# Kernel optimization log

Hardware: AMD Instinct MI355X
Metric: run time of the kernel (lower is better)

## Reference

```python
import jax, jax.numpy as jnp
import numpy as np

C = 128  # in_dim

def _proj(x, w, b):
    # 1x1 conv: x [b,c,h,w], w [out,in], b [out] -> [b,out,h*w]
    bsz, c, h, wd = x.shape
    y = jnp.einsum('bchw,oc->bohw', x, w) + b[None, :, None, None]
    return y.reshape(bsz, -1, h * wd)

def setup_inputs() -> dict:
    key = jax.random.key(0)
    ks = jax.random.split(key, 7)
    x = jax.random.normal(ks[0], (16, C, 128, 128), dtype=jnp.float32)
    s = 1.0 / np.sqrt(C)
    qw = jax.random.normal(ks[1], (C, C), dtype=jnp.float32) * s
    kw = jax.random.normal(ks[2], (C, C), dtype=jnp.float32) * s
    vw = jax.random.normal(ks[3], (C, C), dtype=jnp.float32) * s
    qb = jax.random.normal(ks[4], (C,), dtype=jnp.float32) * 0.01
    kb = jax.random.normal(ks[5], (C,), dtype=jnp.float32) * 0.01
    vb = jax.random.normal(ks[6], (C,), dtype=jnp.float32) * 0.01
    return {'x': x, 'qw': qw, 'qb': qb, 'kw': kw, 'kb': kb, 'vw': vw, 'vb': vb}

def reference(x, qw, qb, kw, kb, vw, vb):
    x_s, x_t = jnp.split(x, 2, axis=0)
    b, c, h, w = x_s.shape
    q_s = _proj(x_s, qw, qb); q_t = _proj(x_t, qw, qb)   # [b,c,N]
    k_s = _proj(x_s, kw, kb); k_t = _proj(x_t, kw, kb)   # [b,c,N]
    v_s = _proj(x_s, vw, vb); v_t = _proj(x_t, vw, vb)   # [b,c,N]
    # channel cross-attentions: contract over spatial N -> [b,c,c]
    a_st = jax.nn.softmax(jnp.einsum('bcn,bdn->bcd', q_t, k_s), axis=-1)
    a_ts = jax.nn.softmax(jnp.einsum('bcn,bdn->bcd', q_s, k_t), axis=-1)
    att = jax.nn.softmax(jnp.einsum('bce,bde->bcd', a_st, a_ts), axis=-1)
    out_s = jnp.einsum('bcd,bdn->bcn', att, v_s).reshape(b, c, h, w)
    out_t = jnp.einsum('bcd,bdn->bcn', att, v_t).reshape(b, c, h, w)
    return jnp.concatenate((x_s + out_s, x_t + out_t), axis=0)
```

## Files before the change

### kernel.cpp

```cpp
#include <hip/hip_runtime.h>
#include <hip/hip_bf16.h>

#define CC 128
#define NSP 16384
#define NFULL (CC * NSP)

typedef float f32x4 __attribute__((ext_vector_type(4)));
typedef short s16x8 __attribute__((ext_vector_type(8)));
typedef unsigned int u32x4 __attribute__((ext_vector_type(4)));

#define GLOAD16(g, l) __builtin_amdgcn_global_load_lds( \
    (const __attribute__((address_space(1))) void*)(g), \
    (__attribute__((address_space(3))) void*)(l), 16, 0, 0)

__device__ __forceinline__ unsigned bf16rne(float f) {
  unsigned u = __float_as_uint(f);
  return ((u + 0x7FFFu + ((u >> 16) & 1u)) >> 16) & 0xFFFFu;
}

__device__ __forceinline__ uint2 packpair(float x0, float x1) {
  __hip_bfloat162 h2 = __float22bfloat162_rn(make_float2(x0, x1));
  unsigned hu = *reinterpret_cast<unsigned*>(&h2);
  float hf0 = __uint_as_float(hu << 16);
  float hf1 = __uint_as_float(hu & 0xFFFF0000u);
  __hip_bfloat162 l2 = __float22bfloat162_rn(make_float2(x0 - hf0, x1 - hf1));
  unsigned lu = *reinterpret_cast<unsigned*>(&l2);
  return make_uint2(hu, lu);
}

__global__ __launch_bounds__(256) void zerok(float* __restrict__ p, int n) {
  int i = blockIdx.x * 256 + threadIdx.x;
  if (i < n) p[i] = 0.f;
}

__global__ __launch_bounds__(256, 2) void k1_mfma(const float* __restrict__ x,
    float* __restrict__ Mdst, float* __restrict__ rs, float* __restrict__ rt,
    float* __restrict__ rspart, float* __restrict__ rtpart,
    int nst, int mode) {
  const int b = blockIdx.y;
  const int chunk = blockIdx.x;
  const int n0 = chunk * (nst * 32);
  const int t = threadIdx.x;
  const int w = t >> 6, l = t & 63;
  const int wr = w >> 1, wc = w & 1;
  const int lr = l & 15, lg = l >> 4;
  __shared__ __align__(16) char LB[2][2][128 * 128];
  const float* Xs = x + (size_t)b * NFULL;
  const float* Xt = x + (size_t)(b + 8) * NFULL;
  const int srow0 = w * 32 + (l >> 3);
  const int sn16x = (l & 7);

  f32x4 acc[4][4];
#pragma unroll
  for (int a = 0; a < 4; ++a)
#pragma unroll
    for (int bb = 0; bb < 4; ++bb) acc[a][bb] = (f32x4){0.f, 0.f, 0.f, 0.f};
  float rtp[4] = {0.f, 0.f, 0.f, 0.f};
  float rsp[4] = {0.f, 0.f, 0.f, 0.f};

  {
#pragma unroll
    for (int i = 0; i < 4; ++i) {
      int row = srow0 + i * 8;
      int n16 = sn16x ^ (row & 7);
      GLOAD16(Xt + (size_t)row * NSP + n0 + n16 * 4, &LB[0][0][(w * 32 + i * 8) * 128]);
      GLOAD16(Xs + (size_t)row * NSP + n0 + n16 * 4, &LB[0][1][(w * 32 + i * 8) * 128]);
    }
  }

  for (int s = 0; s < nst; ++s) {
    const int cur = s & 1;
    __syncthreads();
    if (s + 1 < nst) {
      const int nb = n0 + (s + 1) * 32;
#pragma unroll
      for (int i = 0; i < 4; ++i) {
        int row = srow0 + i * 8;
        int n16 = sn16x ^ (row & 7);
        GLOAD16(Xt + (size_t)row * NSP + nb + n16 * 4, &LB[cur ^ 1][0][(w * 32 + i * 8) * 128]);
        GLOAD16(Xs + (size_t)row * NSP + nb + n16 * 4, &LB[cur ^ 1][1][(w * 32 + i * 8) * 128]);
      }
    }
    const char* A = &LB[cur][0][0];
    const char* B = &LB[cur][1][0];
    s16x8 ah[4], al[4], bh[4], bl[4];
#pragma unroll
    for (int a = 0; a < 4; ++a) {
      int row = wr * 64 + a * 16 + lr;
      int base = row * 128, sw = row & 7;
      f32x4 f0 = *(const f32x4*)(A + base + (((lg * 2) ^ sw) << 4));
      f32x4 f1 = *(const f32x4*)(A + base + (((lg * 2 + 1) ^ sw) << 4));
      rtp[a] += ((f0[0] + f0[1]) + (f0[2] + f0[3])) + ((f1[0] + f1[1]) + (f1[2] + f1[3]));
      uint2 p0 = packpair(f0[0], f0[1]);
      uint2 p1 = packpair(f0[2], f0[3]);
      uint2 p2 = packpair(f1[0], f1[1]);
      uint2 p3 = packpair(f1[2], f1[3]);
      u32x4 H = {p0.x, p1.x, p2.x, p3.x};
      u32x4 L = {p0.y, p1.y, p2.y, p3.y};
      ah[a] = __builtin_bit_cast(s16x8, H);
      al[a] = __builtin_bit_cast(s16x8, L);
    }
#pragma unroll
    for (int bb = 0; bb < 4; ++bb) {
      int row = wc * 64 + bb * 16 + lr;
      int base = row * 128, sw = row & 7;
      f32x4 f0 = *(const f32x4*)(B + base + (((lg * 2) ^ sw) << 4));
      f32x4 f1 = *(const f32x4*)(B + base + (((lg * 2 + 1) ^ sw) << 4));
      rsp[bb] += ((f0[0] + f0[1]) + (f0[2] + f0[3])) + ((f1[0] + f1[1]) + (f1[2] + f1[3]));
      uint2 p0 = packpair(f0[0], f0[1]);
      uint2 p1 = packpair(f0[2], f0[3]);
      uint2 p2 = packpair(f1[0], f1[1]);
      uint2 p3 = packpair(f1[2], f1[3]);
      u32x4 H = {p0.x, p1.x, p2.x, p3.x};
      u32x4 L = {p0.y, p1.y, p2.y, p3.y};
      bh[bb] = __builtin_bit_cast(s16x8, H);
      bl[bb] = __builtin_bit_cast(s16x8, L);
    }
#pragma unroll
    for (int a = 0; a < 4; ++a)
#pragma unroll
      for (int bb = 0; bb < 4; ++bb) {
        acc[a][bb] = __builtin_amdgcn_mfma_f32_16x16x32_bf16(ah[a], bh[bb], acc[a][bb], 0, 0, 0);
        acc[a][bb] = __builtin_amdgcn_mfma_f32_16x16x32_bf16(ah[a], bl[bb], acc[a][bb], 0, 0, 0);
        acc[a][bb] = __builtin_amdgcn_mfma_f32_16x16x32_bf16(al[a], bh[bb], acc[a][bb], 0, 0, 0);
      }
  }

#pragma unroll
  for (int a = 0; a < 4; ++a) {
    float vt = rtp[a];
    vt += __shfl_xor(vt, 16);
    vt += __shfl_xor(vt, 32);
    float vs = rsp[a];
    vs += __shfl_xor(vs, 16);
    vs += __shfl_xor(vs, 32);
    if (l < 16) {
      if (wc == 0) {
        int row = wr * 64 + a * 16 + l;
        if (mode == 0) rtpart[((size_t)chunk * 8 + b) * CC + row] = vt;
        else atomicAdd(&rt[b * CC + row], vt);
      }
      if (wr == 0) {
        int row = wc * 64 + a * 16 + l;
        if (mode == 0) rspart[((size_t)chunk * 8 + b) * CC + row] = vs;
        else atomicAdd(&rs[b * CC + row], vs);
      }
    }
  }

  const int rquad = lg << 2;
  if (mode == 0) {
    float* Mp = Mdst + ((size_t)chunk * 8 + b) * (CC * CC);
#pragma unroll
    for (int a = 0; a < 4; ++a)
#pragma unroll
      for (int bb = 0; bb < 4; ++bb)
#pragma unroll
        for (int r = 0; r < 4; ++r) {
          int i = wr * 64 + a * 16 + rquad + r;
          int j = wc * 64 + bb * 16 + lr;
          Mp[i * CC + j] = acc[a][bb][r];
        }
  } else {
    float* Mp = Mdst + (size_t)b * (CC * CC);
#pragma unroll
    for (int a = 0; a < 4; ++a)
#pragma unroll
      for (int bb = 0; bb < 4; ++bb)
#pragma unroll
        for (int r = 0; r < 4; ++r) {
          int i = wr * 64 + a * 16 + rquad + r;
          int j = wc * 64 + bb * 16 + lr;
          atomicAdd(&Mp[i * CC + j], acc[a][bb][r]);
        }
  }
}

__global__ __launch_bounds__(256) void k1_reduce(const float* __restrict__ Mpart,
    const float* __restrict__ rspart, const float* __restrict__ rtpart,
    float* __restrict__ M, float* __restrict__ rs, float* __restrict__ rt,
    int NB) {
  const int t = threadIdx.x;
  if (blockIdx.x < 128) {
    const int i4 = blockIdx.x * 256 + t;
    const int b = i4 >> 12;
    const int e = (i4 & 4095) * 4;
    f32x4 s = (f32x4){0.f, 0.f, 0.f, 0.f};
    for (int c = 0; c < NB; ++c) {
      f32x4 v = *(const f32x4*)(Mpart + ((size_t)c * 8 + b) * (CC * CC) + e);
      s += v;
    }
    *(f32x4*)(M + (size_t)b * CC * CC + e) = s;
  } else if (blockIdx.x == 128) {
    const int e = t * 4;
    f32x4 s = (f32x4){0.f, 0.f, 0.f, 0.f};
    for (int c = 0; c < NB; ++c) s += *(const f32x4*)(rtpart + (size_t)c * 1024 + e);
    *(f32x4*)(rt + e) = s;
  } else {
    const int e = t * 4;
    f32x4 s = (f32x4){0.f, 0.f, 0.f, 0.f};
    for (int c = 0; c < NB; ++c) s += *(const f32x4*)(rspart + (size_t)c * 1024 + e);
    *(f32x4*)(rs + e) = s;
  }
}

__global__ __launch_bounds__(256) void k2ab(const float* __restrict__ M,
    const float* __restrict__ qw, const float* __restrict__ kw,
    const float* __restrict__ qb, const float* __restrict__ kb,
    const float* __restrict__ rs, const float* __restrict__ rt,
    float* __restrict__ Ast, float* __restrict__ Ats) {
  const int b = blockIdx.y;
  const int c0 = blockIdx.x * 8;
  __shared__ float Big[128][132];
  __shared__ float Wq[8][128];
  __shared__ float T12[2][8][128];
  __shared__ float uvv[2][8];
  __shared__ float wv2[2][128];
  const int t = threadIdx.x;
  const float* Mb = M + (size_t)b * CC * CC;
#pragma unroll
  for (int p = 0; p < 16; ++p) {
    int f = p * 256 + t;
    int row = f >> 5, c4 = (f & 31) * 4;
    *(f32x4*)&Big[row][c4] = *(const f32x4*)(Mb + row * CC + c4);
  }
  { int row = t >> 5, c4 = (t & 31) * 4;
    *(f32x4*)&Wq[row][c4] = *(const f32x4*)(qw + (c0 + row) * CC + c4); }
  __syncthreads();
  if (t < 16) {
    int c = t & 7;
    const float* r = ((t < 8) ? rs : rt) + b * CC;
    float s = 0.f;
    for (int i = 0; i < CC; ++i) s += Wq[c][i] * r[i];
    uvv[(t < 8) ? 1 : 0][c] = s;
  }
  const int tr = t >> 5;
  const int L = t & 31;
  {
    float a1[4] = {0.f, 0.f, 0.f, 0.f}, a2[4] = {0.f, 0.f, 0.f, 0.f};
    for (int i = 0; i < CC; ++i) {
      float wq = Wq[tr][i];
#pragma unroll
      for (int j = 0; j < 4; ++j) a1[j] += wq * Big[i][L + 32 * j];
    }
    for (int i4 = 0; i4 < 32; ++i4) {
      f32x4 wq4 = *(const f32x4*)&Wq[tr][i4 * 4];
#pragma unroll
      for (int j = 0; j < 4; ++j) {
        f32x4 m4 = *(const f32x4*)&Big[L + 32 * j][i4 * 4];
        a2[j] += wq4[0]*m4[0] + wq4[1]*m4[1] + wq4[2]*m4[2] + wq4[3]*m4[3];
      }
    }
#pragma unroll
    for (int j = 0; j < 4; ++j) {
      T12[0][tr][L + 32 * j] = a1[j];
      T12[1][tr][L + 32 * j] = a2[j];
    }
  }
  __syncthreads();
#pragma unroll
  for (int p = 0; p < 16; ++p) {
    int f = p * 256 + t;
    int row = f >> 5, c4 = (f & 31) * 4;
    *(f32x4*)&Big[row][c4] = *(const f32x4*)(kw + row * CC + c4);
  }
  __syncthreads();
  {
    int d = t & 127, wh = t >> 7;
    const float* r = (wh ? rt : rs) + b * CC;
    float s = 0.f;
    for (int i4 = 0; i4 < 32; ++i4) {
      f32x4 w4 = *(const f32x4*)&Big[d][i4 * 4];
      s += w4[0]*r[i4*4] + w4[1]*r[i4*4+1] + w4[2]*r[i4*4+2] + w4[3]*r[i4*4+3];
    }
    wv2[wh][d] = s;
  }
  __syncthreads();
  const int c = c0 + tr;
  const float bqc = qb[c];
#pragma unroll 1
  for (int which = 0; which < 2; ++which) {
    float g[4];
#pragma unroll
    for (int j = 0; j < 4; ++j) {
      int d = L + 32 * j;
      g[j] = uvv[which][tr] * kb[d] + bqc * wv2[which][d] + 16384.f * bqc * kb[d];
    }
    for (int j4 = 0; j4 < 32; ++j4) {
      f32x4 tv4 = *(const f32x4*)&T12[which][tr][j4 * 4];
#pragma unroll
      for (int j = 0; j < 4; ++j) {
        f32x4 w4 = *(const f32x4*)&Big[L + 32 * j][j4 * 4];
        g[j] += tv4[0]*w4[0] + tv4[1]*w4[1] + tv4[2]*w4[2] + tv4[3]*w4[3];
      }
    }
    float m = fmaxf(fmaxf(g[0], g[1]), fmaxf(g[2], g[3]));
#pragma unroll
    for (int off = 1; off < 32; off <<= 1) m = fmaxf(m, __shfl_xor(m, off));
    float s = 0.f;
#pragma unroll
    for (int j = 0; j < 4; ++j) { g[j] = expf(g[j] - m); s += g[j]; }
#pragma unroll
    for (int off = 1; off < 32; off <<= 1) s += __shfl_xor(s, off);
    const float inv = 1.f / s;
    float* A = (which ? Ats : Ast) + (size_t)b * CC * CC + (size_t)c * CC;
#pragma unroll
    for (int j = 0; j < 4; ++j) A[L + 32 * j] = g[j] * inv;
  }
}

__global__ __launch_bounds__(256) void k2cd(const float* __restrict__ Ast,
    const float* __restrict__ Ats, const float* __restrict__ vw,
    const float* __restrict__ vb, unsigned short* __restrict__ Pbf,
    float* __restrict__ c0v) {
  const int b = blockIdx.y;
  const int c0 = blockIdx.x * 8;
  __shared__ float Big[128][132];
  __shared__ float Tl[8][128];
  __shared__ float Al[8][128];
  const int t = threadIdx.x;
  const float* Bb = Ats + (size_t)b * CC * CC;
  const float* Tb = Ast + (size_t)b * CC * CC;
#pragma unroll
  for (int p = 0; p < 16; ++p) {
    int f = p * 256 + t;
    int row = f >> 5, c4 = (f & 31) * 4;
    *(f32x4*)&Big[row][c4] = *(const f32x4*)(Bb + row * CC + c4);
  }
  { int row = t >> 5, c4 = (t & 31) * 4;
    *(f32x4*)&Tl[row][c4] = *(const f32x4*)(Tb + (c0 + row) * CC + c4); }
  __syncthreads();
  const int tr = t >> 5;
  const int L = t & 31;
  {
    float g[4] = {0.f, 0.f, 0.f, 0.f};
    for (int e4 = 0; e4 < 32; ++e4) {
      f32x4 tv4 = *(const f32x4*)&Tl[tr][e4 * 4];
#pragma unroll
      for (int j = 0; j < 4; ++j) {
        f32x4 a4 = *(const f32x4*)&Big[L + 32 * j][e4 * 4];
        g[j] += tv4[0]*a4[0] + tv4[1]*a4[1] + tv4[2]*a4[2] + tv4[3]*a4[3];
      }
    }
    float m = fmaxf(fmaxf(g[0], g[1]), fmaxf(g[2], g[3]));
#pragma unroll
    for (int off = 1; off < 32; off <<= 1) m = fmaxf(m, __shfl_xor(m, off));
    float s = 0.f;
#pragma unroll
    for (int j = 0; j < 4; ++j) { g[j] = expf(g[j] - m); s += g[j]; }
#pragma unroll
    for (int off = 1; off < 32; off <<= 1) s += __shfl_xor(s, off);
    const float inv = 1.f / s;
#pragma unroll
    for (int j = 0; j < 4; ++j) Al[tr][L + 32 * j] = g[j] * inv;
  }
  __syncthreads();
#pragma unroll
  for (int p = 0; p < 16; ++p) {
    int f = p * 256 + t;
    int row = f >> 5, c4 = (f & 31) * 4;
    *(f32x4*)&Big[row][c4] = *(const f32x4*)(vw + row * CC + c4);
  }
  __syncthreads();
  float p4[4] = {0.f, 0.f, 0.f, 0.f};
  for (int d = 0; d < CC; ++d) {
    float av = Al[tr][d];
#pragma unroll
    for (int j = 0; j < 4; ++j) p4[j] += av * Big[d][L + 32 * j];
  }
  float csum = 0.f;
#pragma unroll
  for (int j = 0; j < 4; ++j) csum += Al[tr][L + 32 * j] * vb[L + 32 * j];
#pragma unroll
  for (int off = 1; off < 32; off <<= 1) csum += __shfl_xor(csum, off);
  const int c = c0 + tr;
  if ((c & 31) == L) p4[c >> 5] += 1.0f;
  unsigned short* Pp = Pbf + (size_t)b * CC * CC + (size_t)c * CC;
#pragma unroll
  for (int j = 0; j < 4; ++j) Pp[L + 32 * j] = (unsigned short)bf16rne(p4[j]);
  if (L == 0) c0v[b * CC + c] = csum;
}

__global__ __launch_bounds__(256, 2) void k3_mfma(const float* __restrict__ x,
    const unsigned short* __restrict__ Pbf, const float* __restrict__ c0v,
    float* __restrict__ out) {
  const int im = blockIdx.y;
  const int pb = im & 7;
  const int n0 = blockIdx.x * 256;
  const float* X = x + (size_t)im * NFULL;
  float* O = out + (size_t)im * NFULL;
  __shared__ unsigned short XT[256 * 128];
  __shared__ float c0l[128];
  const int t = threadIdx.x;
  const int w = t >> 6, l = t & 63;
  const int ln = l & 15, lg = l >> 4;
  if (t < 128) c0l[t] = c0v[pb * CC + t];
#pragma unroll
  for (int p = 0; p < 16; ++p) {
    int d0 = 2 * (t >> 4) + 32 * (p & 3);
    int n4 = (t & 15) * 4 + 64 * (p >> 2);
    f32x4 x0 = *(const f32x4*)(X + (size_t)d0 * NSP + n0 + n4);
    f32x4 x1 = *(const f32x4*)(X + (size_t)(d0 + 1) * NSP + n0 + n4);
#pragma unroll
    for (int i = 0; i < 4; ++i) {
      int n = n4 + i;
      __hip_bfloat162 h2 = __float22bfloat162_rn(make_float2(x0[i], x1[i]));
      unsigned pk = *reinterpret_cast<unsigned*>(&h2);
      int g = ((((n & 3) << 1) ^ ((n >> 2) & 7)) << 4);
      int off = (n * 256 + d0 * 2) ^ g;
      *(unsigned*)((char*)XT + off) = pk;
    }
  }
  const unsigned short* Pg0 = Pbf + (size_t)pb * (CC * CC) + (size_t)ln * CC + lg * 8;
  s16x8 Af0[4][4];
#pragma unroll
  for (int a = 0; a < 4; ++a)
#pragma unroll
    for (int kk = 0; kk < 4; ++kk)
      Af0[a][kk] = *(const s16x8*)(Pg0 + a * 16 * CC + kk * 32);
  __syncthreads();

#pragma unroll
  for (int h = 0; h < 2; ++h) {
    s16x8 Af[4][4];
    if (h == 0) {
#pragma unroll
      for (int a = 0; a < 4; ++a)
#pragma unroll
        for (int kk = 0; kk < 4; ++kk) Af[a][kk] = Af0[a][kk];
    } else {
      const unsigned short* Pg = Pg0 + (size_t)64 * CC;
#pragma unroll
      for (int a = 0; a < 4; ++a)
#pragma unroll
        for (int kk = 0; kk < 4; ++kk)
          Af[a][kk] = *(const s16x8*)(Pg + a * 16 * CC + kk * 32);
    }
#pragma unroll
    for (int sub = 0; sub < 4; ++sub) {
      int row = sub * 64 + w * 16 + ln;
      int g = ((((row & 3) << 1) ^ ((row >> 2) & 7)) << 4);
      s16x8 bf[4];
#pragma unroll
      for (int kk = 0; kk < 4; ++kk)
        bf[kk] = *(const s16x8*)((char*)XT + ((row * 256 + kk * 64 + lg * 16) ^ g));
      f32x4 acc[4];
#pragma unroll
      for (int a = 0; a < 4; ++a) acc[a] = (f32x4){0.f, 0.f, 0.f, 0.f};
#pragma unroll
      for (int kk = 0; kk < 4; ++kk)
#pragma unroll
        for (int a = 0; a < 4; ++a)
          acc[a] = __builtin_amdgcn_mfma_f32_16x16x32_bf16(Af[a][kk], bf[kk], acc[a], 0, 0, 0);
      int n = n0 + sub * 64 + w * 16 + ln;
#pragma unroll
      for (int a = 0; a < 4; ++a)
#pragma unroll
        for (int r = 0; r < 4; ++r) {
          int c = h * 64 + a * 16 + lg * 4 + r;
          __builtin_nontemporal_store(acc[a][r] + c0l[c], O + (size_t)c * NSP + n);
        }
    }
  }
}

extern "C" void kernel_launch(void* const* d_in, const int* in_sizes, int n_in,
                              void* d_out, int out_size, void* d_ws, size_t ws_size,
                              hipStream_t stream) {
  (void)in_sizes; (void)n_in; (void)out_size;
  const float* x  = (const float*)d_in[0];
  const float* qw = (const float*)d_in[1];
  const float* qb = (const float*)d_in[2];
  const float* kw = (const float*)d_in[3];
  const float* kb = (const float*)d_in[4];
  const float* vw = (const float*)d_in[5];
  const float* vb = (const float*)d_in[6];
  float* out = (float*)d_out;
  float* ws = (float*)d_ws;
  float* M   = ws;
  float* rs  = M + 131072;
  float* rt  = rs + 1024;
  float* AST = rt + 1024;
  float* ATS = AST + 131072;
  unsigned short* Pbf = (unsigned short*)(ATS + 131072);
  float* c0v = ATS + 131072 + 65536;
  float* Mpart = c0v + 1024;
  const size_t base_floats = (size_t)(Mpart - ws);

  int NB, mode;
  if (ws_size >= (base_floats + (size_t)32 * (131072 + 2048)) * 4) { NB = 32; mode = 0; }
  else { NB = 32; mode = 1; }
  const int nst = (16384 / NB) / 32;
  float* rtpart = Mpart + (size_t)NB * 131072;
  float* rspart = rtpart + (size_t)NB * 1024;

  if (mode == 1) zerok<<<(133120 + 255) / 256, 256, 0, stream>>>(M, 133120);
  k1_mfma<<<dim3(NB, 8), 256, 0, stream>>>(x, mode ? M : Mpart, rs, rt,
                                           rspart, rtpart, nst, mode);
  if (mode == 0)
    k1_reduce<<<130, 256, 0, stream>>>(Mpart, rspart, rtpart, M, rs, rt, NB);
  k2ab<<<dim3(16, 8), 256, 0, stream>>>(M, qw, kw, qb, kb, rs, rt, AST, ATS);
  k2cd<<<dim3(16, 8), 256, 0, stream>>>(AST, ATS, vw, vb, Pbf, c0v);
  k3_mfma<<<dim3(64, 16), 256, 0, stream>>>(x, Pbf, c0v, out);
}
```

Before: 137.2 us.

## Halve rows per block in k2ab/k2cd and vectorize k3 output stores via swapped MFMA

k2ab and k2cd now handle 4 channel rows per block instead of 8, using 64 lanes per row and doubling the grid to 256 blocks so more CUs are busy in these small stages. Each block still loads the full 128x128 matrices, so total global and LDS traffic for those loads doubles. Separately, k3_mfma swaps the MFMA operand order so each lane holds 4 consecutive spatial outputs for one channel. This lets the output be written with one 16-byte nontemporal vector store per accumulator instead of four scalar stores.

```diff
diff --git a/kernel.cpp b/kernel.cpp
--- a/kernel.cpp
+++ b/kernel.cpp
@@ -210,11 +210,11 @@
     const float* __restrict__ rs, const float* __restrict__ rt,
     float* __restrict__ Ast, float* __restrict__ Ats) {
   const int b = blockIdx.y;
-  const int c0 = blockIdx.x * 8;
+  const int c0 = blockIdx.x * 4;
   __shared__ float Big[128][132];
-  __shared__ float Wq[8][128];
-  __shared__ float T12[2][8][128];
-  __shared__ float uvv[2][8];
+  __shared__ float Wq[4][128];
+  __shared__ float T12[2][4][128];
+  __shared__ float uvv[2][4];
   __shared__ float wv2[2][128];
   const int t = threadIdx.x;
   const float* Mb = M + (size_t)b * CC * CC;
@@ -224,37 +224,39 @@
     int row = f >> 5, c4 = (f & 31) * 4;
     *(f32x4*)&Big[row][c4] = *(const f32x4*)(Mb + row * CC + c4);
   }
-  { int row = t >> 5, c4 = (t & 31) * 4;
-    *(f32x4*)&Wq[row][c4] = *(const f32x4*)(qw + (c0 + row) * CC + c4); }
-  __syncthreads();
-  if (t < 16) {
-    int c = t & 7;
-    const float* r = ((t < 8) ? rs : rt) + b * CC;
+  if (t < 128) {
+    int row = t >> 5, c4 = (t & 31) * 4;
+    *(f32x4*)&Wq[row][c4] = *(const f32x4*)(qw + (c0 + row) * CC + c4);
+  }
+  __syncthreads();
+  if (t < 8) {
+    int c = t & 3;
+    const float* r = ((t < 4) ? rs : rt) + b * CC;
     float s = 0.f;
     for (int i = 0; i < CC; ++i) s += Wq[c][i] * r[i];
-    uvv[(t < 8) ? 1 : 0][c] = s;
-  }
-  const int tr = t >> 5;
-  const int L = t & 31;
+    uvv[(t < 4) ? 1 : 0][c] = s;
+  }
+  const int tr = t >> 6;
+  const int L = t & 63;
   {
-    float a1[4] = {0.f, 0.f, 0.f, 0.f}, a2[4] = {0.f, 0.f, 0.f, 0.f};
+    float a1[2] = {0.f, 0.f}, a2[2] = {0.f, 0.f};
     for (int i = 0; i < CC; ++i) {
       float wq = Wq[tr][i];
 #pragma unroll
-      for (int j = 0; j < 4; ++j) a1[j] += wq * Big[i][L + 32 * j];
+      for (int j = 0; j < 2; ++j) a1[j] += wq * Big[i][L + 64 * j];
     }
     for (int i4 = 0; i4 < 32; ++i4) {
       f32x4 wq4 = *(const f32x4*)&Wq[tr][i4 * 4];
 #pragma unroll
-      for (int j = 0; j < 4; ++j) {
-        f32x4 m4 = *(const f32x4*)&Big[L + 32 * j][i4 * 4];
+      for (int j = 0; j < 2; ++j) {
+        f32x4 m4 = *(const f32x4*)&Big[L + 64 * j][i4 * 4];
         a2[j] += wq4[0]*m4[0] + wq4[1]*m4[1] + wq4[2]*m4[2] + wq4[3]*m4[3];
       }
     }
 #pragma unroll
-    for (int j = 0; j < 4; ++j) {
-      T12[0][tr][L + 32 * j] = a1[j];
-      T12[1][tr][L + 32 * j] = a2[j];
+    for (int j = 0; j < 2; ++j) {
+      T12[0][tr][L + 64 * j] = a1[j];
+      T12[1][tr][L + 64 * j] = a2[j];
     }
   }
   __syncthreads();
@@ -280,32 +282,31 @@
   const float bqc = qb[c];
 #pragma unroll 1
   for (int which = 0; which < 2; ++which) {
-    float g[4];
-#pragma unroll
-    for (int j = 0; j < 4; ++j) {
-      int d = L + 32 * j;
+    float g[2];
+#pragma unroll
+    for (int j = 0; j < 2; ++j) {
+      int d = L + 64 * j;
       g[j] = uvv[which][tr] * kb[d] + bqc * wv2[which][d] + 16384.f * bqc * kb[d];
     }
     for (int j4 = 0; j4 < 32; ++j4) {
       f32x4 tv4 = *(const f32x4*)&T12[which][tr][j4 * 4];
 #pragma unroll
-      for (int j = 0; j < 4; ++j) {
-        f32x4 w4 = *(const f32x4*)&Big[L + 32 * j][j4 * 4];
+      for (int j = 0; j < 2; ++j) {
+        f32x4 w4 = *(const f32x4*)&Big[L + 64 * j][j4 * 4];
         g[j] += tv4[0]*w4[0] + tv4[1]*w4[1] + tv4[2]*w4[2] + tv4[3]*w4[3];
       }
     }
-    float m = fmaxf(fmaxf(g[0], g[1]), fmaxf(g[2], g[3]));
-#pragma unroll
-    for (int off = 1; off < 32; off <<= 1) m = fmaxf(m, __shfl_xor(m, off));
-    float s = 0.f;
-#pragma unroll
-    for (int j = 0; j < 4; ++j) { g[j] = expf(g[j] - m); s += g[j]; }
-#pragma unroll
-    for (int off = 1; off < 32; off <<= 1) s += __shfl_xor(s, off);
+    float m = fmaxf(g[0], g[1]);
+#pragma unroll
+    for (int off = 1; off < 64; off <<= 1) m = fmaxf(m, __shfl_xor(m, off));
+    float s = g[0] = expf(g[0] - m);
+    s += (g[1] = expf(g[1] - m));
+#pragma unroll
+    for (int off = 1; off < 64; off <<= 1) s += __shfl_xor(s, off);
     const float inv = 1.f / s;
     float* A = (which ? Ats : Ast) + (size_t)b * CC * CC + (size_t)c * CC;
-#pragma unroll
-    for (int j = 0; j < 4; ++j) A[L + 32 * j] = g[j] * inv;
+    A[L] = g[0] * inv;
+    A[L + 64] = g[1] * inv;
   }
 }
 
@@ -314,10 +315,10 @@
     const float* __restrict__ vb, unsigned short* __restrict__ Pbf,
     float* __restrict__ c0v) {
   const int b = blockIdx.y;
-  const int c0 = blockIdx.x * 8;
+  const int c0 = blockIdx.x * 4;
   __shared__ float Big[128][132];
-  __shared__ float Tl[8][128];
-  __shared__ float Al[8][128];
+  __shared__ float Tl[4][128];
+  __shared__ float Al[4][128];
   const int t = threadIdx.x;
   const float* Bb = Ats + (size_t)b * CC * CC;
   const float* Tb = Ast + (size_t)b * CC * CC;
@@ -327,32 +328,33 @@
     int row = f >> 5, c4 = (f & 31) * 4;
     *(f32x4*)&Big[row][c4] = *(const f32x4*)(Bb + row * CC + c4);
   }
-  { int row = t >> 5, c4 = (t & 31) * 4;
-    *(f32x4*)&Tl[row][c4] = *(const f32x4*)(Tb + (c0 + row) * CC + c4); }
-  __syncthreads();
-  const int tr = t >> 5;
-  const int L = t & 31;
+  if (t < 128) {
+    int row = t >> 5, c4 = (t & 31) * 4;
+    *(f32x4*)&Tl[row][c4] = *(const f32x4*)(Tb + (c0 + row) * CC + c4);
+  }
+  __syncthreads();
+  const int tr = t >> 6;
+  const int L = t & 63;
   {
-    float g[4] = {0.f, 0.f, 0.f, 0.f};
+    float g[2] = {0.f, 0.f};
     for (int e4 = 0; e4 < 32; ++e4) {
       f32x4 tv4 = *(const f32x4*)&Tl[tr][e4 * 4];
 #pragma unroll
-      for (int j = 0; j < 4; ++j) {
-        f32x4 a4 = *(const f32x4*)&Big[L + 32 * j][e4 * 4];
+      for (int j = 0; j < 2; ++j) {
+        f32x4 a4 = *(const f32x4*)&Big[L + 64 * j][e4 * 4];
         g[j] += tv4[0]*a4[0] + tv4[1]*a4[1] + tv4[2]*a4[2] + tv4[3]*a4[3];
       }
     }
-    float m = fmaxf(fmaxf(g[0], g[1]), fmaxf(g[2], g[3]));
-#pragma unroll
-    for (int off = 1; off < 32; off <<= 1) m = fmaxf(m, __shfl_xor(m, off));
-    float s = 0.f;
-#pragma unroll
-    for (int j = 0; j < 4; ++j) { g[j] = expf(g[j] - m); s += g[j]; }
-#pragma unroll
-    for (int off = 1; off < 32; off <<= 1) s += __shfl_xor(s, off);
+    float m = fmaxf(g[0], g[1]);
+#pragma unroll
+    for (int off = 1; off < 64; off <<= 1) m = fmaxf(m, __shfl_xor(m, off));
+    float s = g[0] = expf(g[0] - m);
+    s += (g[1] = expf(g[1] - m));
+#pragma unroll
+    for (int off = 1; off < 64; off <<= 1) s += __shfl_xor(s, off);
     const float inv = 1.f / s;
-#pragma unroll
-    for (int j = 0; j < 4; ++j) Al[tr][L + 32 * j] = g[j] * inv;
+    Al[tr][L] = g[0] * inv;
+    Al[tr][L + 64] = g[1] * inv;
   }
   __syncthreads();
 #pragma unroll
@@ -362,22 +364,20 @@
     *(f32x4*)&Big[row][c4] = *(const f32x4*)(vw + row * CC + c4);
   }
   __syncthreads();
-  float p4[4] = {0.f, 0.f, 0.f, 0.f};
+  float p2[2] = {0.f, 0.f};
   for (int d = 0; d < CC; ++d) {
     float av = Al[tr][d];
 #pragma unroll
-    for (int j = 0; j < 4; ++j) p4[j] += av * Big[d][L + 32 * j];
-  }
-  float csum = 0.f;
-#pragma unroll
-  for (int j = 0; j < 4; ++j) csum += Al[tr][L + 32 * j] * vb[L + 32 * j];
-#pragma unroll
-  for (int off = 1; off < 32; off <<= 1) csum += __shfl_xor(csum, off);
+    for (int j = 0; j < 2; ++j) p2[j] += av * Big[d][L + 64 * j];
+  }
+  float csum = Al[tr][L] * vb[L] + Al[tr][L + 64] * vb[L + 64];
+#pragma unroll
+  for (int off = 1; off < 64; off <<= 1) csum += __shfl_xor(csum, off);
   const int c = c0 + tr;
-  if ((c & 31) == L) p4[c >> 5] += 1.0f;
+  if ((c & 63) == L) p2[c >> 6] += 1.0f;
   unsigned short* Pp = Pbf + (size_t)b * CC * CC + (size_t)c * CC;
-#pragma unroll
-  for (int j = 0; j < 4; ++j) Pp[L + 32 * j] = (unsigned short)bf16rne(p4[j]);
+  Pp[L] = (unsigned short)bf16rne(p2[0]);
+  Pp[L + 64] = (unsigned short)bf16rne(p2[1]);
   if (L == 0) c0v[b * CC + c] = csum;
 }
 
@@ -451,15 +451,16 @@
       for (int kk = 0; kk < 4; ++kk)
 #pragma unroll
         for (int a = 0; a < 4; ++a)
-          acc[a] = __builtin_amdgcn_mfma_f32_16x16x32_bf16(Af[a][kk], bf[kk], acc[a], 0, 0, 0);
-      int n = n0 + sub * 64 + w * 16 + ln;
-#pragma unroll
-      for (int a = 0; a < 4; ++a)
-#pragma unroll
-        for (int r = 0; r < 4; ++r) {
-          int c = h * 64 + a * 16 + lg * 4 + r;
-          __builtin_nontemporal_store(acc[a][r] + c0l[c], O + (size_t)c * NSP + n);
-        }
+          acc[a] = __builtin_amdgcn_mfma_f32_16x16x32_bf16(bf[kk], Af[a][kk], acc[a], 0, 0, 0);
+      int nbase = n0 + sub * 64 + w * 16 + lg * 4;
+#pragma unroll
+      for (int a = 0; a < 4; ++a) {
+        int c = h * 64 + a * 16 + ln;
+        float cc0 = c0l[c];
+        f32x4 r = acc[a];
+        r[0] += cc0; r[1] += cc0; r[2] += cc0; r[3] += cc0;
+        __builtin_nontemporal_store(r, (f32x4*)(O + (size_t)c * NSP + nbase));
+      }
     }
   }
 }
@@ -499,7 +500,7 @@
                                            rspart, rtpart, nst, mode);
   if (mode == 0)
     k1_reduce<<<130, 256, 0, stream>>>(Mpart, rspart, rtpart, M, rs, rt, NB);
-  k2ab<<<dim3(16, 8), 256, 0, stream>>>(M, qw, kw, qb, kb, rs, rt, AST, ATS);
-  k2cd<<<dim3(16, 8), 256, 0, stream>>>(AST, ATS, vw, vb, Pbf, c0v);
+  k2ab<<<dim3(32, 8), 256, 0, stream>>>(M, qw, kw, qb, kb, rs, rt, AST, ATS);
+  k2cd<<<dim3(32, 8), 256, 0, stream>>>(AST, ATS, vw, vb, Pbf, c0v);
   k3_mfma<<<dim3(64, 16), 256, 0, stream>>>(x, Pbf, c0v, out);
 }
```

Result: faster. 125.7 us, median of 2 (-8.4%).
